# Performance work log

Hardware: AMD Instinct MI355X
Metric: run time of the kernel (lower is better)

## Reference

```python
import jax, jax.numpy as jnp
import numpy as np

B, N, D_IN, D_HID, N_ITER = 32, 512, 256, 128, 10


def setup_inputs() -> dict:
    key = jax.random.key(0)
    ks = jax.random.split(key, 8)
    s = 1.0 / np.sqrt(D_IN)  # torch Linear default init range
    return {
        "Xh": jax.random.normal(ks[0], (B, N, D_IN), jnp.float32),
        "Xm": jax.random.normal(ks[1], (B, N, D_IN), jnp.float32),
        # position 0 is the root; tokens 1..len are valid
        "lengths": jax.random.randint(ks[2], (B,), N // 2, N),
        "Wh": jax.random.uniform(ks[3], (D_HID, D_IN), jnp.float32, -s, s),
        "bh": jax.random.uniform(ks[4], (D_HID,), jnp.float32, -s, s),
        "Wm": jax.random.uniform(ks[5], (D_HID, D_IN), jnp.float32, -s, s),
        "bm": jax.random.uniform(ks[6], (D_HID,), jnp.float32, -s, s),
        "V": 0.01 * jax.random.normal(ks[7], (D_HID, D_HID), jnp.float32),
    }


def _logZ(scores, lengths):
    """Matrix-tree log-partition for single-root nonprojective trees.

    scores: [B,N,N] arc scores, scores[b,h,m] = head h -> modifier m, index 0 = root.
    lengths: [B] number of real tokens (valid modifiers at 1..len).
    """
    Bn, Nn, _ = scores.shape
    idx = jnp.arange(Nn)
    tok = (idx[None, :] >= 1) & (idx[None, :] <= lengths[:, None])   # [B,N] valid modifiers
    head = idx[None, :] <= lengths[:, None]                          # [B,N] valid heads (incl. root)
    pair = head[:, :, None] & tok[:, None, :] & (idx[:, None] != idx[None, :])
    # stability shift: every tree has exactly `len` edges, so logZ shifts by len*c
    c = jax.lax.stop_gradient(
        jnp.max(jnp.where(pair, scores, -jnp.inf), axis=(1, 2)))
    A = jnp.where(pair, jnp.exp(scores - c[:, None, None]), 0.0)     # [B,N,N]
    r = A[:, 0, 1:]                                                  # root -> token weights [B,N-1]
    At = A[:, 1:, 1:]                                                # token -> token weights
    ar = jnp.arange(Nn - 1)
    # Laplacian L = diag(colsum) - At (diag of At is zero by pair mask)
    Lap = (-At).at[:, ar, ar].set(r + At.sum(axis=1))
    # Koo et al. (2007): replace first row with root weights
    Lhat = Lap.at[:, 0, :].set(r)
    # padded positions: identity rows to keep det unchanged
    Lhat = Lhat.at[:, ar, ar].add(jnp.where(tok[:, 1:], 0.0, 1.0))
    _, logabs = jnp.linalg.slogdet(Lhat)
    return logabs + lengths.astype(scores.dtype) * c


def _marginals(scores, lengths):
    """nonprojective_marginals: (logZ, entropy, mu) via grad of logZ."""
    def f(s):
        lz = _logZ(s, lengths)
        return lz.sum(), lz
    (_, logZ), Y = jax.value_and_grad(f, has_aux=True)(scores)
    entr = logZ - jnp.sum(Y * scores, axis=(1, 2))
    return logZ, entr, Y


def reference(Xh, Xm, lengths, Wh, bh, Wm, bm, V):
    # dropout=0 -> H_mask/M_mask are ones
    H0 = Xh @ Wh.T + bh          # h_mlp(Xh), invariant across iterations
    M0 = Xm @ Wm.T + bm          # m_mlp(Xm)
    H = jax.nn.relu(H0)
    M = jax.nn.relu(M0)
    scores = jnp.einsum("bhu,uv,bmv->bhm", H, V, M)
    logZ, entr, Y = _marginals(scores, lengths)
    for _ in range(1, N_ITER):
        Hn = jax.nn.relu(H0 + Y @ M @ V.T)                       # _update_H
        Mn = jax.nn.relu(M0 + jnp.swapaxes(Y, -2, -1) @ H @ V)   # _update_M
        scores = jnp.einsum("bhu,uv,bmv->bhm", Hn, V, Mn)
        logZ, entr, Y = _marginals(scores, lengths)
        H, M = Hn, Mn
    return scores, logZ, Y, entr
```

## Files before the change

### kernel.cpp

```cpp
#include <hip/hip_runtime.h>
#include <math.h>

constexpr int BB = 32;
constexpr int NN_ = 512;
constexpr int DIN = 256;
constexpr int DH = 128;
constexpr int NITER = 10;
constexpr long HSTR = (long)NN_ * DH;
constexpr long SSTR = (long)NN_ * NN_;
constexpr long LSTR = 512L * 512L;

__device__ __forceinline__ unsigned f2mono(float f) {
    unsigned u = __float_as_uint(f);
    return (u & 0x80000000u) ? ~u : (u | 0x80000000u);
}
__device__ __forceinline__ float mono2f(unsigned u) {
    return __uint_as_float((u & 0x80000000u) ? (u & 0x7fffffffu) : ~u);
}

__device__ __forceinline__ float invert128(float r[8][8], int tid,
        float (*RowP)[8][132], float (*ColPT)[8][132], float (*Rnew)[8][132])
{
    int tx = tid & 15, ty = tid >> 4;
    int lane = tid & 63, w = tid >> 6;
    int li = lane >> 3, lj = lane & 7;
    const bool act = (tid < 256);
    float lacc = 0.f;
    __syncthreads();
    for (int s8 = 0; s8 < 16; ++s8) {
        int p = s8 & 1;
        if (act && ty == s8) {
            #pragma unroll
            for (int i = 0; i < 8; ++i)
                #pragma unroll
                for (int j = 0; j < 8; ++j)
                    RowP[p][i][tx * 8 + j] = r[i][j];
        }
        if (act && tx == s8) {
            float sub = (ty == s8) ? 1.f : 0.f;
            #pragma unroll
            for (int i = 0; i < 8; ++i)
                #pragma unroll
                for (int j = 0; j < 8; ++j)
                    ColPT[p][j][ty * 8 + i] = r[i][j] - ((i == j) ? sub : 0.f);
        }
        __syncthreads();
        float d = RowP[p][li][s8 * 8 + lj];
        float prod = 1.f;
        #pragma unroll
        for (int s = 0; s < 8; ++s) {
            float pv = __shfl(d, s * 9);
            prod *= pv;
            float pinv = 1.0f / pv;
            float rv = __shfl(d, s * 8 + lj);
            float cv = __shfl(d, li * 8 + s);
            float nd;
            if (li == s && lj == s)  nd = pinv;
            else if (li == s)        nd = rv * pinv;
            else if (lj == s)        nd = -cv * pinv;
            else                     nd = d - cv * pinv * rv;
            d = nd;
        }
        lacc += logf(fabsf(prod));
        if (act) {
            int sr = li;
            int jq = w * 32 + lj * 4;
            float dsr[8];
            #pragma unroll
            for (int t = 0; t < 8; ++t) dsr[t] = __shfl(d, (lane & 56) + t);
            float a0 = 0.f, a1 = 0.f, a2 = 0.f, a3 = 0.f;
            #pragma unroll
            for (int t = 0; t < 8; ++t) {
                float4 rp = *(const float4*)&RowP[p][t][jq];
                a0 += dsr[t] * rp.x; a1 += dsr[t] * rp.y;
                a2 += dsr[t] * rp.z; a3 += dsr[t] * rp.w;
            }
            if ((jq >> 3) == s8) {
                if ((jq & 7) == 0) {
                    a0 = dsr[0] + ((sr == 0) ? 1.f : 0.f);
                    a1 = dsr[1] + ((sr == 1) ? 1.f : 0.f);
                    a2 = dsr[2] + ((sr == 2) ? 1.f : 0.f);
                    a3 = dsr[3] + ((sr == 3) ? 1.f : 0.f);
                } else {
                    a0 = dsr[4] + ((sr == 4) ? 1.f : 0.f);
                    a1 = dsr[5] + ((sr == 5) ? 1.f : 0.f);
                    a2 = dsr[6] + ((sr == 6) ? 1.f : 0.f);
                    a3 = dsr[7] + ((sr == 7) ? 1.f : 0.f);
                }
            }
            *(float4*)&Rnew[p][sr][jq] = make_float4(a0, a1, a2, a3);
        }
        __syncthreads();
        if (act) {
            #pragma unroll
            for (int t = 0; t < 8; ++t) {
                float cp[8], rn[8];
                *(float4*)&cp[0] = *(const float4*)&ColPT[p][t][ty * 8];
                *(float4*)&cp[4] = *(const float4*)&ColPT[p][t][ty * 8 + 4];
                *(float4*)&rn[0] = *(const float4*)&Rnew[p][t][tx * 8];
                *(float4*)&rn[4] = *(const float4*)&Rnew[p][t][tx * 8 + 4];
                #pragma unroll
                for (int i = 0; i < 8; ++i)
                    #pragma unroll
                    for (int j = 0; j < 8; ++j)
                        r[i][j] -= cp[i] * rn[j];
            }
        }
    }
    return lacc;
}

template<int AMODE, int BMODE, int EPI>
__global__ __launch_bounds__(256) void gemm64(
    const float* __restrict__ A, const float* __restrict__ Bm,
    float* __restrict__ C, const float* __restrict__ Dp, float* __restrict__ C2,
    int Mdim, int Ndim, int Kdim,
    long sA, long sB, long sC, long sD)
{
    constexpr int BK = 16;
    __shared__ float As[BK][64 + 4];
    __shared__ float Bs[BK][64 + 4];
    int b = blockIdx.z;
    const float* Ab = A + (long)b * sA;
    const float* Bb = Bm + (long)b * sB;
    int m0 = blockIdx.x * 64, n0 = blockIdx.y * 64;
    int tid = threadIdx.x;
    int tx = tid & 15, ty = tid >> 4;
    float acc[4][4] = {};

    int arow, acol, brow, bcol;
    if (AMODE == 0) { arow = tid >> 2; acol = (tid & 3) * 4; }
    else            { arow = tid >> 4; acol = (tid & 15) * 4; }
    if (BMODE == 0) { brow = tid >> 4; bcol = (tid & 15) * 4; }
    else            { brow = tid >> 2; bcol = (tid & 3) * 4; }

    float4 av, bv;
    if (AMODE == 0) av = *(const float4*)(Ab + (long)(m0 + arow) * Kdim + acol);
    else            av = *(const float4*)(Ab + (long)(0 + arow) * Mdim + m0 + acol);
    if (BMODE == 0) bv = *(const float4*)(Bb + (long)(0 + brow) * Ndim + n0 + bcol);
    else            bv = *(const float4*)(Bb + (long)(n0 + brow) * Kdim + bcol);

    for (int k0 = 0; k0 < Kdim; k0 += BK) {
        __syncthreads();
        if (AMODE == 0) {
            As[acol + 0][arow] = av.x; As[acol + 1][arow] = av.y;
            As[acol + 2][arow] = av.z; As[acol + 3][arow] = av.w;
        } else {
            *(float4*)&As[arow][acol] = av;
        }
        if (BMODE == 0) {
            *(float4*)&Bs[brow][bcol] = bv;
        } else {
            Bs[bcol + 0][brow] = bv.x; Bs[bcol + 1][brow] = bv.y;
            Bs[bcol + 2][brow] = bv.z; Bs[bcol + 3][brow] = bv.w;
        }
        float4 av2, bv2;
        if (k0 + BK < Kdim) {
            int k1 = k0 + BK;
            if (AMODE == 0) av2 = *(const float4*)(Ab + (long)(m0 + arow) * Kdim + k1 + acol);
            else            av2 = *(const float4*)(Ab + (long)(k1 + arow) * Mdim + m0 + acol);
            if (BMODE == 0) bv2 = *(const float4*)(Bb + (long)(k1 + brow) * Ndim + n0 + bcol);
            else            bv2 = *(const float4*)(Bb + (long)(n0 + brow) * Kdim + k1 + bcol);
        }
        __syncthreads();
        #pragma unroll
        for (int k = 0; k < BK; ++k) {
            float4 a4 = *(const float4*)&As[k][ty * 4];
            float4 b4 = *(const float4*)&Bs[k][tx * 4];
            float avv[4] = {a4.x, a4.y, a4.z, a4.w};
            float bvv[4] = {b4.x, b4.y, b4.z, b4.w};
            #pragma unroll
            for (int i = 0; i < 4; ++i)
                #pragma unroll
                for (int j = 0; j < 4; ++j)
                    acc[i][j] += avv[i] * bvv[j];
        }
        av = av2; bv = bv2;
    }

    int r0 = m0 + ty * 4, c0 = n0 + tx * 4;
    if (EPI == 0) {
        float* Cb = C + (long)b * sC;
        #pragma unroll
        for (int i = 0; i < 4; ++i)
            *(float4*)(Cb + (long)(r0 + i) * Ndim + c0) =
                make_float4(acc[i][0], acc[i][1], acc[i][2], acc[i][3]);
    } else if (EPI == 1) {
        float4 bias = *(const float4*)(Dp + c0);
        float bb4[4] = {bias.x, bias.y, bias.z, bias.w};
        #pragma unroll
        for (int i = 0; i < 4; ++i) {
            float pre[4];
            #pragma unroll
            for (int j = 0; j < 4; ++j) pre[j] = acc[i][j] + bb4[j];
            *(float4*)(C2 + (long)(r0 + i) * Ndim + c0) =
                make_float4(pre[0], pre[1], pre[2], pre[3]);
            *(float4*)(C + (long)(r0 + i) * Ndim + c0) =
                make_float4(fmaxf(pre[0], 0.f), fmaxf(pre[1], 0.f),
                            fmaxf(pre[2], 0.f), fmaxf(pre[3], 0.f));
        }
    } else {
        const float* Db = Dp + (long)b * sD;
        float* Cb = C + (long)b * sC;
        #pragma unroll
        for (int i = 0; i < 4; ++i) {
            float4 d = *(const float4*)(Db + (long)(r0 + i) * Ndim + c0);
            float pre[4] = {acc[i][0] + d.x, acc[i][1] + d.y,
                            acc[i][2] + d.z, acc[i][3] + d.w};
            *(float4*)(Cb + (long)(r0 + i) * Ndim + c0) =
                make_float4(fmaxf(pre[0], 0.f), fmaxf(pre[1], 0.f),
                            fmaxf(pre[2], 0.f), fmaxf(pre[3], 0.f));
        }
    }
}

__global__ __launch_bounds__(256) void score_gemm(
    const float* __restrict__ A, const float* __restrict__ Bm,
    float* __restrict__ C, const int* __restrict__ len,
    unsigned* __restrict__ cu)
{
    int b = blockIdx.z;
    const float* Ab = A + (long)b * HSTR;
    const float* Bb = Bm + (long)b * HSTR;
    int m0 = blockIdx.x * 128, n0 = blockIdx.y * 128;
    int tid = threadIdx.x, tx = tid & 15, ty = tid >> 4;
    __shared__ float As[8][132];
    __shared__ float Bs[8][132];
    float acc[8][8] = {};
    int row = tid >> 1, kq = (tid & 1) << 2;
    float4 av = *(const float4*)(Ab + (long)(m0 + row) * DH + kq);
    float4 bv = *(const float4*)(Bb + (long)(n0 + row) * DH + kq);
    for (int kc = 0; kc < DH; kc += 8) {
        __syncthreads();
        As[kq + 0][row] = av.x; As[kq + 1][row] = av.y;
        As[kq + 2][row] = av.z; As[kq + 3][row] = av.w;
        Bs[kq + 0][row] = bv.x; Bs[kq + 1][row] = bv.y;
        Bs[kq + 2][row] = bv.z; Bs[kq + 3][row] = bv.w;
        float4 av2, bv2;
        if (kc + 8 < DH) {
            av2 = *(const float4*)(Ab + (long)(m0 + row) * DH + kc + 8 + kq);
            bv2 = *(const float4*)(Bb + (long)(n0 + row) * DH + kc + 8 + kq);
        }
        __syncthreads();
        #pragma unroll
        for (int k = 0; k < 8; ++k) {
            float a[8], bb[8];
            *(float4*)&a[0] = *(float4*)&As[k][ty * 8];
            *(float4*)&a[4] = *(float4*)&As[k][ty * 8 + 4];
            *(float4*)&bb[0] = *(float4*)&Bs[k][tx * 8];
            *(float4*)&bb[4] = *(float4*)&Bs[k][tx * 8 + 4];
            #pragma unroll
            for (int i = 0; i < 8; ++i)
                #pragma unroll
                for (int j = 0; j < 8; ++j) acc[i][j] += a[i] * bb[j];
        }
        av = av2; bv = bv2;
    }
    int L = len[b];
    float vmax = -3.0e38f;
    float* Cb = C + (long)b * SSTR;
    #pragma unroll
    for (int i = 0; i < 8; ++i) {
        int h = m0 + ty * 8 + i;
        bool hok = (h <= L);
        *(float4*)(Cb + (long)h * NN_ + n0 + tx * 8) =
            make_float4(acc[i][0], acc[i][1], acc[i][2], acc[i][3]);
        *(float4*)(Cb + (long)h * NN_ + n0 + tx * 8 + 4) =
            make_float4(acc[i][4], acc[i][5], acc[i][6], acc[i][7]);
        #pragma unroll
        for (int j = 0; j < 8; ++j) {
            int m = n0 + tx * 8 + j;
            if (hok && m >= 1 && m <= L && m != h) vmax = fmaxf(vmax, acc[i][j]);
        }
    }
    __syncthreads();
    float* red = &As[0][0];
    red[tid] = vmax; __syncthreads();
    for (int off = 128; off; off >>= 1) {
        if (tid < off) red[tid] = fmaxf(red[tid], red[tid + off]);
        __syncthreads();
    }
    if (tid == 0) atomicMax(&cu[b], f2mono(red[0]));
}

__global__ void zero_scal(float* scal) {
    if (threadIdx.x < 224) scal[threadIdx.x] = 0.f;
}

__global__ __launch_bounds__(256) void colsum_k(const float* __restrict__ sc,
                                                const int* __restrict__ len,
                                                const unsigned* __restrict__ cu,
                                                float* __restrict__ colsum)
{
    int b = blockIdx.x, yb = blockIdx.y;
    int tid = threadIdx.x, lane = tid & 63, w = tid >> 6;
    int L = len[b];
    float c = mono2f(cu[b]);
    int m = yb * 64 + lane;
    const float* S = sc + (long)b * SSTR;
    float s = 0.f;
    bool mv = (m >= 1 && m <= L);
    if (mv) {
        for (int h = 1 + w; h < NN_; h += 4) {
            if (h <= L && h != m) s += expf(S[(long)h * NN_ + m] - c);
        }
    }
    __shared__ float part[4][64];
    part[w][lane] = s; __syncthreads();
    if (tid < 64)
        colsum[(long)b * NN_ + yb * 64 + tid] =
            part[0][tid] + part[1][tid] + part[2][tid] + part[3][tid];
}

__global__ __launch_bounds__(256) void build_rows(const float* __restrict__ sc,
                                                  const int* __restrict__ len,
                                                  const unsigned* __restrict__ cu,
                                                  const float* __restrict__ colsum,
                                                  float* __restrict__ Lm,
                                                  float* __restrict__ Fb0,
                                                  float* __restrict__ logdet)
{
    __shared__ float sm[6][8][132];
    int b = blockIdx.x;
    int tid = threadIdx.x;
    int L = len[b];
    float c = mono2f(cu[b]);
    const float* S = sc + (long)b * SSTR;
    const float* cs = colsum + (long)b * NN_;

    if (blockIdx.y == 0) {
        int tx = tid & 15, ty = tid >> 4;
        float r[8][8];
        #pragma unroll
        for (int i = 0; i < 8; ++i) {
            int gi = ty * 8 + i;
            #pragma unroll
            for (int j = 0; j < 8; ++j) {
                int gj = tx * 8 + j;
                int tm = gj + 1;
                bool mv = (tm <= L);
                float v;
                if (gi == 0) {
                    v = mv ? expf(S[tm] - c) : 0.f;
                } else if (gi == gj) {
                    float rv = mv ? expf(S[tm] - c) : 0.f;
                    v = rv + cs[tm] + (mv ? 0.f : 1.f);
                } else {
                    int h = gi + 1;
                    v = (h <= L && mv) ? -expf(S[(long)h * NN_ + tm] - c) : 0.f;
                }
                r[i][j] = v;
            }
        }
        float lacc = invert128(r, tid,
                               (float(*)[8][132])&sm[0],
                               (float(*)[8][132])&sm[2],
                               (float(*)[8][132])&sm[4]);
        float* Ab = Lm + (long)b * LSTR;
        #pragma unroll
        for (int i = 0; i < 8; ++i) {
            *(float4*)(Ab + (long)(ty * 8 + i) * 512 + tx * 8) =
                make_float4(r[i][0], r[i][1], r[i][2], r[i][3]);
            *(float4*)(Ab + (long)(ty * 8 + i) * 512 + tx * 8 + 4) =
                make_float4(r[i][4], r[i][5], r[i][6], r[i][7]);
        }
        if (tid == 0) atomicAdd(&logdet[b], lacc);
        return;
    }

    int i0 = (blockIdx.y - 1) * 8;
    #pragma unroll
    for (int r = 0; r < 8; ++r) {
        int i = i0 + r;
        float* Lrow = Lm + (long)b * LSTR + (long)i * 512;
        float* Frow = Fb0 + (long)b * HSTR + (long)i * 128;
        #pragma unroll
        for (int q = 0; q < 2; ++q) {
            int j = tid + q * 256;
            float v;
            if (i == 511 || j == 511) {
                v = (i == j) ? 1.f : 0.f;
            } else {
                int tm = j + 1;
                bool mv = (tm <= L);
                if (i == 0) {
                    v = mv ? expf(S[tm] - c) : 0.f;
                } else if (i == j) {
                    float rv = mv ? expf(S[tm] - c) : 0.f;
                    v = rv + cs[tm] + ((tm > L) ? 1.f : 0.f);
                } else {
                    int h = i + 1;
                    v = (h <= L && mv) ? -expf(S[(long)h * NN_ + tm] - c) : 0.f;
                }
            }
            if (!(i < 128 && j < 128)) Lrow[j] = v;
            if (q == 0 && j < 128 && i >= 128) Frow[j] = v;
        }
    }
}

__global__ __launch_bounds__(256) void gj_panel(float* __restrict__ Lm,
                                                float* __restrict__ Fnext, int kb)
{
    constexpr int BK = 16;
    __shared__ float Ds[BK][132];
    __shared__ float As2[BK][36];
    int b = blockIdx.x;
    int j = blockIdx.y >> 2;
    int cq = blockIdx.y & 3;
    int jt = j + (j >= kb);
    int c0 = cq * 32;
    int tid = threadIdx.x;
    int tx = tid & 7, ty = tid >> 3;
    float* base = Lm + (long)b * LSTR;
    const float* D = base + (long)(kb * 128) * 512 + kb * 128;
    float* Aj = base + (long)(kb * 128) * 512 + jt * 128;
    int drow = tid >> 1, dk8 = (tid & 1) * 8;
    int akr = tid >> 3, acq4 = (tid & 7) * 4;
    bool aload = (akr < BK);
    float acc[4][4] = {};
    float4 dva = *(const float4*)(D + (long)drow * 512 + dk8);
    float4 dvb = *(const float4*)(D + (long)drow * 512 + dk8 + 4);
    float4 av;
    if (aload) av = *(const float4*)(Aj + (long)akr * 512 + c0 + acq4);
    for (int kc = 0; kc < 128; kc += BK) {
        __syncthreads();
        Ds[dk8 + 0][drow] = dva.x; Ds[dk8 + 1][drow] = dva.y;
        Ds[dk8 + 2][drow] = dva.z; Ds[dk8 + 3][drow] = dva.w;
        Ds[dk8 + 4][drow] = dvb.x; Ds[dk8 + 5][drow] = dvb.y;
        Ds[dk8 + 6][drow] = dvb.z; Ds[dk8 + 7][drow] = dvb.w;
        if (aload) *(float4*)&As2[akr][acq4] = av;
        float4 dva2, dvb2, av2;
        if (kc + BK < 128) {
            dva2 = *(const float4*)(D + (long)drow * 512 + kc + BK + dk8);
            dvb2 = *(const float4*)(D + (long)drow * 512 + kc + BK + dk8 + 4);
            if (aload) av2 = *(const float4*)(Aj + (long)(kc + BK + akr) * 512 + c0 + acq4);
        }
        __syncthreads();
        #pragma unroll
        for (int k = 0; k < BK; ++k) {
            float4 a4 = *(const float4*)&Ds[k][ty * 4];
            float4 b4 = *(const float4*)&As2[k][tx * 4];
            float a[4] = {a4.x, a4.y, a4.z, a4.w};
            float bb[4] = {b4.x, b4.y, b4.z, b4.w};
            #pragma unroll
            for (int i = 0; i < 4; ++i)
                #pragma unroll
                for (int jj = 0; jj < 4; ++jj)
                    acc[i][jj] += a[i] * bb[jj];
        }
        dva = dva2; dvb = dvb2; av = av2;
    }
    bool dual = (jt == kb + 1);
    float* Fn = Fnext + (long)b * HSTR + (long)(kb * 128) * 128;
    #pragma unroll
    for (int i = 0; i < 4; ++i) {
        float4 o = make_float4(acc[i][0], acc[i][1], acc[i][2], acc[i][3]);
        *(float4*)(Aj + (long)(ty * 4 + i) * 512 + c0 + tx * 4) = o;
        if (dual) *(float4*)(Fn + (long)(ty * 4 + i) * 128 + c0 + tx * 4) = o;
    }
}

__global__ __launch_bounds__(256) void gj_update64(
    float* __restrict__ Lm, const float* __restrict__ Fbuf,
    float* __restrict__ Fnext, float* __restrict__ logdet,
    unsigned* __restrict__ cnt, int kb)
{
    constexpr int BK = 16;
    __shared__ float sm[6 * 8 * 132];
    int b = blockIdx.x;
    int tid = threadIdx.x;

    if (blockIdx.z == 0) {
        if (blockIdx.y != 0 || kb >= 3) return;
        if (tid == 0) {
            while (__hip_atomic_load(&cnt[kb * 32 + b], __ATOMIC_ACQUIRE,
                                     __HIP_MEMORY_SCOPE_AGENT) < 4u) {}
        }
        __syncthreads();
        int tx = tid & 15, ty = tid >> 4;
        float* Dd = Lm + (long)b * LSTR + (long)((kb + 1) * 128) * 512 + (kb + 1) * 128;
        float r[8][8];
        #pragma unroll
        for (int i = 0; i < 8; ++i) {
            *(float4*)&r[i][0] = *(const float4*)(Dd + (long)(ty * 8 + i) * 512 + tx * 8);
            *(float4*)&r[i][4] = *(const float4*)(Dd + (long)(ty * 8 + i) * 512 + tx * 8 + 4);
        }
        float lacc = invert128(r, tid,
                               (float(*)[8][132])sm,
                               (float(*)[8][132])(sm + 2 * 8 * 132),
                               (float(*)[8][132])(sm + 4 * 8 * 132));
        #pragma unroll
        for (int i = 0; i < 8; ++i) {
            *(float4*)(Dd + (long)(ty * 8 + i) * 512 + tx * 8) =
                make_float4(r[i][0], r[i][1], r[i][2], r[i][3]);
            *(float4*)(Dd + (long)(ty * 8 + i) * 512 + tx * 8 + 4) =
                make_float4(r[i][4], r[i][5], r[i][6], r[i][7]);
        }
        if (tid == 0) atomicAdd(&logdet[b], lacc);
        return;
    }

    float (*Fs)[68] = (float (*)[68])sm;
    float (*Rs)[68] = (float (*)[68])(sm + BK * 68);
    int il = blockIdx.y;
    int it = (kb < 3) ? ((il == 0) ? kb : (il == kb ? 0 : il)) : il;
    int ib = it + (it >= kb);
    int sub = blockIdx.z - 1;
    int jl = sub >> 2;
    int jt = (kb < 3) ? ((jl == 0) ? kb + 1 : (jl == kb + 1 ? 0 : jl)) : jl;
    int quad = sub & 3;
    int r0 = (quad >> 1) * 64, c0 = (quad & 1) * 64;
    int tx = tid & 15, ty = tid >> 4;
    float* base = Lm + (long)b * LSTR;
    const float* F = Fbuf + (long)b * HSTR + (long)(ib * 128 + r0) * 128;
    const float* R = base + (long)(kb * 128) * 512 + jt * 128 + c0;
    float* Cb = base + (long)(ib * 128 + r0) * 512 + jt * 128 + c0;
    int frow = tid >> 2, fkq = (tid & 3) << 2;
    int rkr = tid >> 4, rcq = (tid & 15) << 2;
    float acc[4][4] = {};
    float4 fv = *(const float4*)(F + (long)frow * 128 + fkq);
    float4 rv = *(const float4*)(R + (long)rkr * 512 + rcq);
    for (int kc = 0; kc < 128; kc += BK) {
        __syncthreads();
        Fs[fkq + 0][frow] = fv.x; Fs[fkq + 1][frow] = fv.y;
        Fs[fkq + 2][frow] = fv.z; Fs[fkq + 3][frow] = fv.w;
        *(float4*)&Rs[rkr][rcq] = rv;
        float4 fv2, rv2;
        if (kc + BK < 128) {
            fv2 = *(const float4*)(F + (long)frow * 128 + kc + BK + fkq);
            rv2 = *(const float4*)(R + (long)(kc + BK + rkr) * 512 + rcq);
        }
        __syncthreads();
        #pragma unroll
        for (int k = 0; k < BK; ++k) {
            float4 a4 = *(const float4*)&Fs[k][ty * 4];
            float4 b4 = *(const float4*)&Rs[k][tx * 4];
            float a[4] = {a4.x, a4.y, a4.z, a4.w};
            float bb[4] = {b4.x, b4.y, b4.z, b4.w};
            #pragma unroll
            for (int i = 0; i < 4; ++i)
                #pragma unroll
                for (int j = 0; j < 4; ++j)
                    acc[i][j] += a[i] * bb[j];
        }
        fv = fv2; rv = rv2;
    }
    bool dual = (jt == kb + 1);
    float* Fn = Fnext + (long)b * HSTR + (long)(ib * 128 + r0) * 128 + c0;
    if (jt == kb) {
        #pragma unroll
        for (int i = 0; i < 4; ++i)
            *(float4*)(Cb + (long)(ty * 4 + i) * 512 + tx * 4) =
                make_float4(-acc[i][0], -acc[i][1], -acc[i][2], -acc[i][3]);
    } else {
        #pragma unroll
        for (int i = 0; i < 4; ++i) {
            float4 o = *(const float4*)(Cb + (long)(ty * 4 + i) * 512 + tx * 4);
            o = make_float4(o.x - acc[i][0], o.y - acc[i][1],
                            o.z - acc[i][2], o.w - acc[i][3]);
            *(float4*)(Cb + (long)(ty * 4 + i) * 512 + tx * 4) = o;
            if (dual) *(float4*)(Fn + (long)(ty * 4 + i) * 128 + tx * 4) = o;
        }
    }
    if (kb < 3 && ib == kb + 1 && jt == kb + 1) {
        __threadfence();
        __syncthreads();
        if (tid == 0)
            __hip_atomic_fetch_add(&cnt[kb * 32 + b], 1u, __ATOMIC_RELEASE,
                                   __HIP_MEMORY_SCOPE_AGENT);
    }
}

__global__ __launch_bounds__(256) void y_k(const float* __restrict__ sc,
                                           const float* __restrict__ Binv,
                                           const int* __restrict__ len,
                                           const unsigned* __restrict__ cu,
                                           float* __restrict__ Y,
                                           float* __restrict__ Ssum)
{
    int b = blockIdx.x;
    int ht = blockIdx.y >> 3, mt = blockIdx.y & 7;
    int h0 = ht * 64, m0 = mt * 64;
    int tid = threadIdx.x;
    int L = len[b];
    float c = mono2f(cu[b]);
    const float* S = sc + (long)b * SSTR;
    const float* Bi = Binv + (long)b * LSTR;
    float* Yb = Y + (long)b * SSTR;
    __shared__ float Bs[64][65];
    __shared__ float Ds[64], C0s[64];
    {
        int hh = tid & 63, m4 = tid >> 6;
        int col = h0 + hh - 1;
        for (int mm = m4; mm < 64; mm += 4) {
            int row = m0 + mm - 1;
            Bs[mm][hh] = (row >= 0 && col >= 0) ? Bi[(long)row * 512 + col] : 0.f;
        }
    }
    if (tid < 64) {
        int row = m0 + tid - 1;
        Ds[tid] = (row >= 0) ? Bi[(long)row * 512 + row] : 0.f;
    } else if (tid < 128) {
        int mm = tid - 64, row = m0 + mm - 1;
        C0s[mm] = (row >= 0) ? Bi[(long)row * 512] : 0.f;
    }
    __syncthreads();
    int mm = tid & 63, hq = tid >> 6;
    int m = m0 + mm;
    float lsum = 0.f;
    bool mvalid = (m >= 1 && m <= L);
    float dterm = (m >= 2) ? Ds[mm] : 0.f;
    #pragma unroll
    for (int hi = 0; hi < 16; ++hi) {
        int hh = hq * 16 + hi;
        int h = h0 + hh;
        float s = S[(long)h * NN_ + m];
        float y = 0.f;
        if (mvalid && h <= L && h != m) {
            float a = expf(s - c);
            float g;
            if (h == 0) g = C0s[mm] + dterm;
            else g = dterm - ((h >= 2) ? Bs[mm][hh] : 0.f);
            y = a * g;
        }
        Yb[(long)h * NN_ + m] = y;
        lsum += y * s;
    }
    __shared__ float red[256];
    red[tid] = lsum; __syncthreads();
    for (int off = 128; off; off >>= 1) {
        if (tid < off) red[tid] += red[tid + off];
        __syncthreads();
    }
    if (tid == 0) atomicAdd(&Ssum[b], red[0]);
}

__global__ void fin_k(const int* __restrict__ len, unsigned* __restrict__ cu,
                      float* __restrict__ logdet, float* __restrict__ Ssum,
                      unsigned* __restrict__ cnt,
                      float* __restrict__ outLogZ, float* __restrict__ outEntr)
{
    int b = threadIdx.x;
    if (b < 32) {
        float c = mono2f(cu[b]);
        float lz = logdet[b] + (float)len[b] * c;
        outLogZ[b] = lz;
        outEntr[b] = lz - Ssum[b];
        cu[b] = 0u;
        logdet[b] = 0.f;
        Ssum[b] = 0.f;
        cnt[b] = 0u;
        cnt[32 + b] = 0u;
        cnt[64 + b] = 0u;
        cnt[96 + b] = 0u;
    }
}

extern "C" void kernel_launch(void* const* d_in, const int* in_sizes, int n_in,
                              void* d_out, int out_size, void* d_ws, size_t ws_size,
                              hipStream_t stream)
{
    const float* Xh = (const float*)d_in[0];
    const float* Xm = (const float*)d_in[1];
    const int*   len = (const int*)d_in[2];
    const float* Wh = (const float*)d_in[3];
    const float* bh = (const float*)d_in[4];
    const float* Wm = (const float*)d_in[5];
    const float* bm = (const float*)d_in[6];
    const float* V  = (const float*)d_in[7];

    float* ws = (float*)d_ws;
    constexpr long U = 2097152;
    float* H0 = ws;
    float* M0 = ws + U;
    float* Ha = ws + 2 * U;
    float* Ma = ws + 3 * U;
    float* Hb = ws + 4 * U;
    float* Mb = ws + 5 * U;
    float* T1 = ws + 6 * U;
    float* Yt = ws + 7 * U;
    float* Lm = ws + 8 * U;
    float* cs = ws + 12 * U;
    float* scal = ws + 12 * U + 16384;
    unsigned* cu = (unsigned*)scal;
    float* logdet = scal + 32;
    float* Ssum = scal + 64;
    unsigned* cnt = (unsigned*)(scal + 96);

    float* Sout = (float*)d_out;
    float* outLogZ = (float*)d_out + 8388608;
    float* Yout = (float*)d_out + 8388640;
    float* outEntr = (float*)d_out + 8388640 + 8388608;

    zero_scal<<<1, 256, 0, stream>>>(scal);

    gemm64<0,1,1><<<dim3(256, 2, 1), 256, 0, stream>>>(
        Xh, Wh, Ha, bh, H0, 16384, DH, DIN, 0, 0, 0, 0);
    gemm64<0,1,1><<<dim3(256, 2, 1), 256, 0, stream>>>(
        Xm, Wm, Ma, bm, M0, 16384, DH, DIN, 0, 0, 0, 0);

    float* Hc = Ha; float* Mc = Ma; float* Hn = Hb; float* Mn = Mb;
    for (int t = 0; t < NITER; ++t) {
        if (t > 0) {
            gemm64<0,1,0><<<dim3(8,2,BB),256,0,stream>>>(
                Mc, V, Yt, nullptr, nullptr, 512, DH, DH, HSTR, 0, HSTR, 0);
            gemm64<0,0,2><<<dim3(8,2,BB),256,0,stream>>>(
                Yout, Yt, Hn, H0, nullptr, 512, DH, 512, SSTR, HSTR, HSTR, HSTR);
            gemm64<1,0,2><<<dim3(8,2,BB),256,0,stream>>>(
                Yout, T1, Mn, M0, nullptr, 512, DH, 512, SSTR, HSTR, HSTR, HSTR);
            { float* tmp = Hc; Hc = Hn; Hn = tmp; }
            { float* tmp = Mc; Mc = Mn; Mn = tmp; }
        }
        gemm64<0,0,0><<<dim3(8,2,BB),256,0,stream>>>(
            Hc, V, T1, nullptr, nullptr, 512, DH, DH, HSTR, 0, HSTR, 0);
        score_gemm<<<dim3(4,4,BB),256,0,stream>>>(T1, Mc, Sout, len, cu);

        colsum_k<<<dim3(BB,8),256,0,stream>>>(Sout, len, cu, cs);
        build_rows<<<dim3(BB,65),256,0,stream>>>(Sout, len, cu, cs, Lm, Yt, logdet);

        float* Fbufs[2] = {Yt, Hn};
        for (int kb = 0; kb < 4; ++kb) {
            float* Fcur  = Fbufs[kb & 1];
            float* Fnext = Fbufs[(kb + 1) & 1];
            gj_panel<<<dim3(BB,12),256,0,stream>>>(Lm, Fnext, kb);
            gj_update64<<<dim3(BB,3,17),256,0,stream>>>(Lm, Fcur, Fnext, logdet, cnt, kb);
        }
        y_k<<<dim3(BB,64),256,0,stream>>>(Sout, Lm, len, cu, Yout, Ssum);
        fin_k<<<1,32,0,stream>>>(len, cu, logdet, Ssum, cnt, outLogZ, outEntr);
    }
}
```

Measured before the change: 5.861 ms.

## Remove spin-wait sync in GJ update, self-compute next diag block; add 32-row update GEMM

The block-Gauss-Jordan update kernel no longer spin-waits on an atomic counter for the next diagonal tile. Instead, a dedicated block recomputes that tile itself (a 128x128x128 GEMM subtract) and then inverts it, while the other blocks skip it. The diagonal-0 build is split into its own kernel, and the H/M update GEMMs switch to a smaller 32x64 tile kernel for more blocks. This removes inter-block busy-waiting and its counters, but one block per batch now does a serial GEMM plus inversion that may sit on the critical path.

```diff
diff --git a/kernel.cpp b/kernel.cpp
--- a/kernel.cpp
+++ b/kernel.cpp
@@ -214,6 +214,86 @@
     }
 }
 
+template<int AMODE>
+__global__ __launch_bounds__(256) void gemm32(
+    const float* __restrict__ A, const float* __restrict__ Bm,
+    float* __restrict__ C, const float* __restrict__ Dp,
+    int Mdim, int Ndim, int Kdim,
+    long sA, long sB, long sC, long sD)
+{
+    constexpr int BK = 16;
+    __shared__ float As[BK][36];
+    __shared__ float Bs[BK][68];
+    int b = blockIdx.z;
+    const float* Ab = A + (long)b * sA;
+    const float* Bb = Bm + (long)b * sB;
+    int m0 = blockIdx.x * 32, n0 = blockIdx.y * 64;
+    int tid = threadIdx.x;
+    int tx = tid & 15, ty = tid >> 4;
+    float acc[2][4] = {};
+
+    int arow, acol;
+    if (AMODE == 0) { arow = tid >> 2; acol = (tid & 3) * 4; }
+    else            { arow = tid >> 3; acol = (tid & 7) * 4; }
+    bool aload = (tid < 128);
+    int brow = tid >> 4, bcol = (tid & 15) * 4;
+
+    float4 av, bv;
+    if (aload) {
+        if (AMODE == 0) av = *(const float4*)(Ab + (long)(m0 + arow) * Kdim + acol);
+        else            av = *(const float4*)(Ab + (long)arow * Mdim + m0 + acol);
+    }
+    bv = *(const float4*)(Bb + (long)brow * Ndim + n0 + bcol);
+
+    for (int k0 = 0; k0 < Kdim; k0 += BK) {
+        __syncthreads();
+        if (aload) {
+            if (AMODE == 0) {
+                As[acol + 0][arow] = av.x; As[acol + 1][arow] = av.y;
+                As[acol + 2][arow] = av.z; As[acol + 3][arow] = av.w;
+            } else {
+                *(float4*)&As[arow][acol] = av;
+            }
+        }
+        *(float4*)&Bs[brow][bcol] = bv;
+        float4 av2, bv2;
+        if (k0 + BK < Kdim) {
+            int k1 = k0 + BK;
+            if (aload) {
+                if (AMODE == 0) av2 = *(const float4*)(Ab + (long)(m0 + arow) * Kdim + k1 + acol);
+                else            av2 = *(const float4*)(Ab + (long)(k1 + arow) * Mdim + m0 + acol);
+            }
+            bv2 = *(const float4*)(Bb + (long)(k1 + brow) * Ndim + n0 + bcol);
+        }
+        __syncthreads();
+        #pragma unroll
+        for (int k = 0; k < BK; ++k) {
+            float a0 = As[k][ty * 2], a1 = As[k][ty * 2 + 1];
+            float4 b4 = *(const float4*)&Bs[k][tx * 4];
+            float bb[4] = {b4.x, b4.y, b4.z, b4.w};
+            #pragma unroll
+            for (int j = 0; j < 4; ++j) {
+                acc[0][j] += a0 * bb[j];
+                acc[1][j] += a1 * bb[j];
+            }
+        }
+        av = av2; bv = bv2;
+    }
+
+    int r0 = m0 + ty * 2, c0 = n0 + tx * 4;
+    const float* Db = Dp + (long)b * sD;
+    float* Cb = C + (long)b * sC;
+    #pragma unroll
+    for (int i = 0; i < 2; ++i) {
+        float4 d = *(const float4*)(Db + (long)(r0 + i) * Ndim + c0);
+        float pre[4] = {acc[i][0] + d.x, acc[i][1] + d.y,
+                        acc[i][2] + d.z, acc[i][3] + d.w};
+        *(float4*)(Cb + (long)(r0 + i) * Ndim + c0) =
+            make_float4(fmaxf(pre[0], 0.f), fmaxf(pre[1], 0.f),
+                        fmaxf(pre[2], 0.f), fmaxf(pre[3], 0.f));
+    }
+}
+
 __global__ __launch_bounds__(256) void score_gemm(
     const float* __restrict__ A, const float* __restrict__ Bm,
     float* __restrict__ C, const int* __restrict__ len,
@@ -284,7 +364,7 @@
 }
 
 __global__ void zero_scal(float* scal) {
-    if (threadIdx.x < 224) scal[threadIdx.x] = 0.f;
+    if (threadIdx.x < 96) scal[threadIdx.x] = 0.f;
 }
 
 __global__ __launch_bounds__(256) void colsum_k(const float* __restrict__ sc,
@@ -312,13 +392,12 @@
             part[0][tid] + part[1][tid] + part[2][tid] + part[3][tid];
 }
 
-__global__ __launch_bounds__(256) void build_rows(const float* __restrict__ sc,
-                                                  const int* __restrict__ len,
-                                                  const unsigned* __restrict__ cu,
-                                                  const float* __restrict__ colsum,
-                                                  float* __restrict__ Lm,
-                                                  float* __restrict__ Fb0,
-                                                  float* __restrict__ logdet)
+__global__ __launch_bounds__(256) void build_diag0(const float* __restrict__ sc,
+                                                   const int* __restrict__ len,
+                                                   const unsigned* __restrict__ cu,
+                                                   const float* __restrict__ colsum,
+                                                   float* __restrict__ Lm,
+                                                   float* __restrict__ logdet)
 {
     __shared__ float sm[6][8][132];
     int b = blockIdx.x;
@@ -327,48 +406,59 @@
     float c = mono2f(cu[b]);
     const float* S = sc + (long)b * SSTR;
     const float* cs = colsum + (long)b * NN_;
-
-    if (blockIdx.y == 0) {
-        int tx = tid & 15, ty = tid >> 4;
-        float r[8][8];
-        #pragma unroll
-        for (int i = 0; i < 8; ++i) {
-            int gi = ty * 8 + i;
-            #pragma unroll
-            for (int j = 0; j < 8; ++j) {
-                int gj = tx * 8 + j;
-                int tm = gj + 1;
-                bool mv = (tm <= L);
-                float v;
-                if (gi == 0) {
-                    v = mv ? expf(S[tm] - c) : 0.f;
-                } else if (gi == gj) {
-                    float rv = mv ? expf(S[tm] - c) : 0.f;
-                    v = rv + cs[tm] + (mv ? 0.f : 1.f);
-                } else {
-                    int h = gi + 1;
-                    v = (h <= L && mv) ? -expf(S[(long)h * NN_ + tm] - c) : 0.f;
-                }
-                r[i][j] = v;
-            }
-        }
-        float lacc = invert128(r, tid,
-                               (float(*)[8][132])&sm[0],
-                               (float(*)[8][132])&sm[2],
-                               (float(*)[8][132])&sm[4]);
-        float* Ab = Lm + (long)b * LSTR;
-        #pragma unroll
-        for (int i = 0; i < 8; ++i) {
-            *(float4*)(Ab + (long)(ty * 8 + i) * 512 + tx * 8) =
-                make_float4(r[i][0], r[i][1], r[i][2], r[i][3]);
-            *(float4*)(Ab + (long)(ty * 8 + i) * 512 + tx * 8 + 4) =
-                make_float4(r[i][4], r[i][5], r[i][6], r[i][7]);
-        }
-        if (tid == 0) atomicAdd(&logdet[b], lacc);
-        return;
-    }
-
-    int i0 = (blockIdx.y - 1) * 8;
+    int tx = tid & 15, ty = tid >> 4;
+    float r[8][8];
+    #pragma unroll
+    for (int i = 0; i < 8; ++i) {
+        int gi = ty * 8 + i;
+        #pragma unroll
+        for (int j = 0; j < 8; ++j) {
+            int gj = tx * 8 + j;
+            int tm = gj + 1;
+            bool mv = (tm <= L);
+            float v;
+            if (gi == 0) {
+                v = mv ? expf(S[tm] - c) : 0.f;
+            } else if (gi == gj) {
+                float rv = mv ? expf(S[tm] - c) : 0.f;
+                v = rv + cs[tm] + (mv ? 0.f : 1.f);
+            } else {
+                int h = gi + 1;
+                v = (h <= L && mv) ? -expf(S[(long)h * NN_ + tm] - c) : 0.f;
+            }
+            r[i][j] = v;
+        }
+    }
+    float lacc = invert128(r, tid,
+                           (float(*)[8][132])&sm[0],
+                           (float(*)[8][132])&sm[2],
+                           (float(*)[8][132])&sm[4]);
+    float* Ab = Lm + (long)b * LSTR;
+    #pragma unroll
+    for (int i = 0; i < 8; ++i) {
+        *(float4*)(Ab + (long)(ty * 8 + i) * 512 + tx * 8) =
+            make_float4(r[i][0], r[i][1], r[i][2], r[i][3]);
+        *(float4*)(Ab + (long)(ty * 8 + i) * 512 + tx * 8 + 4) =
+            make_float4(r[i][4], r[i][5], r[i][6], r[i][7]);
+    }
+    if (tid == 0) atomicAdd(&logdet[b], lacc);
+}
+
+__global__ __launch_bounds__(256) void build_rows(const float* __restrict__ sc,
+                                                  const int* __restrict__ len,
+                                                  const unsigned* __restrict__ cu,
+                                                  const float* __restrict__ colsum,
+                                                  float* __restrict__ Lm,
+                                                  float* __restrict__ Fb0)
+{
+    int b = blockIdx.x;
+    int tid = threadIdx.x;
+    int L = len[b];
+    float c = mono2f(cu[b]);
+    const float* S = sc + (long)b * SSTR;
+    const float* cs = colsum + (long)b * NN_;
+
+    int i0 = blockIdx.y * 8;
     #pragma unroll
     for (int r = 0; r < 8; ++r) {
         int i = i0 + r;
@@ -463,39 +553,80 @@
 
 __global__ __launch_bounds__(256) void gj_update64(
     float* __restrict__ Lm, const float* __restrict__ Fbuf,
-    float* __restrict__ Fnext, float* __restrict__ logdet,
-    unsigned* __restrict__ cnt, int kb)
+    float* __restrict__ Fnext, float* __restrict__ logdet, int kb)
 {
     constexpr int BK = 16;
     __shared__ float sm[6 * 8 * 132];
     int b = blockIdx.x;
     int tid = threadIdx.x;
+    float* base = Lm + (long)b * LSTR;
 
     if (blockIdx.z == 0) {
         if (blockIdx.y != 0 || kb >= 3) return;
-        if (tid == 0) {
-            while (__hip_atomic_load(&cnt[kb * 32 + b], __ATOMIC_ACQUIRE,
-                                     __HIP_MEMORY_SCOPE_AGENT) < 4u) {}
-        }
-        __syncthreads();
+        int dt = kb + 1;
+        const float* F = Fbuf + (long)b * HSTR + (long)(dt * 128) * 128;
+        const float* R = base + (long)(kb * 128) * 512 + dt * 128;
+        float* Cb = base + (long)(dt * 128) * 512 + dt * 128;
+        float (*Fs)[132] = (float (*)[132])sm;
+        float (*Rs)[132] = (float (*)[132])(sm + 16 * 132);
         int tx = tid & 15, ty = tid >> 4;
-        float* Dd = Lm + (long)b * LSTR + (long)((kb + 1) * 128) * 512 + (kb + 1) * 128;
-        float r[8][8];
+        int frow = tid >> 1, fkq = (tid & 1) << 3;
+        int rkr = tid >> 4, rcq = (tid & 15) << 3;
+        float acc[8][8] = {};
+        float4 fva = *(const float4*)(F + (long)frow * 128 + fkq);
+        float4 fvb = *(const float4*)(F + (long)frow * 128 + fkq + 4);
+        float4 rva = *(const float4*)(R + (long)rkr * 512 + rcq);
+        float4 rvb = *(const float4*)(R + (long)rkr * 512 + rcq + 4);
+        for (int kc = 0; kc < 128; kc += BK) {
+            __syncthreads();
+            Fs[fkq + 0][frow] = fva.x; Fs[fkq + 1][frow] = fva.y;
+            Fs[fkq + 2][frow] = fva.z; Fs[fkq + 3][frow] = fva.w;
+            Fs[fkq + 4][frow] = fvb.x; Fs[fkq + 5][frow] = fvb.y;
+            Fs[fkq + 6][frow] = fvb.z; Fs[fkq + 7][frow] = fvb.w;
+            *(float4*)&Rs[rkr][rcq] = rva;
+            *(float4*)&Rs[rkr][rcq + 4] = rvb;
+            float4 fva2, fvb2, rva2, rvb2;
+            if (kc + BK < 128) {
+                fva2 = *(const float4*)(F + (long)frow * 128 + kc + BK + fkq);
+                fvb2 = *(const float4*)(F + (long)frow * 128 + kc + BK + fkq + 4);
+                rva2 = *(const float4*)(R + (long)(kc + BK + rkr) * 512 + rcq);
+                rvb2 = *(const float4*)(R + (long)(kc + BK + rkr) * 512 + rcq + 4);
+            }
+            __syncthreads();
+            #pragma unroll
+            for (int k = 0; k < BK; ++k) {
+                float a[8], bb[8];
+                *(float4*)&a[0] = *(const float4*)&Fs[k][ty * 8];
+                *(float4*)&a[4] = *(const float4*)&Fs[k][ty * 8 + 4];
+                *(float4*)&bb[0] = *(const float4*)&Rs[k][tx * 8];
+                *(float4*)&bb[4] = *(const float4*)&Rs[k][tx * 8 + 4];
+                #pragma unroll
+                for (int i = 0; i < 8; ++i)
+                    #pragma unroll
+                    for (int j = 0; j < 8; ++j)
+                        acc[i][j] += a[i] * bb[j];
+            }
+            fva = fva2; fvb = fvb2; rva = rva2; rvb = rvb2;
+        }
         #pragma unroll
         for (int i = 0; i < 8; ++i) {
-            *(float4*)&r[i][0] = *(const float4*)(Dd + (long)(ty * 8 + i) * 512 + tx * 8);
-            *(float4*)&r[i][4] = *(const float4*)(Dd + (long)(ty * 8 + i) * 512 + tx * 8 + 4);
-        }
-        float lacc = invert128(r, tid,
-                               (float(*)[8][132])sm,
-                               (float(*)[8][132])(sm + 2 * 8 * 132),
-                               (float(*)[8][132])(sm + 4 * 8 * 132));
+            float4 o0 = *(const float4*)(Cb + (long)(ty * 8 + i) * 512 + tx * 8);
+            float4 o1 = *(const float4*)(Cb + (long)(ty * 8 + i) * 512 + tx * 8 + 4);
+            acc[i][0] = o0.x - acc[i][0]; acc[i][1] = o0.y - acc[i][1];
+            acc[i][2] = o0.z - acc[i][2]; acc[i][3] = o0.w - acc[i][3];
+            acc[i][4] = o1.x - acc[i][4]; acc[i][5] = o1.y - acc[i][5];
+            acc[i][6] = o1.z - acc[i][6]; acc[i][7] = o1.w - acc[i][7];
+        }
+        float lacc = invert128(acc, tid,
+                               (float (*)[8][132])sm,
+                               (float (*)[8][132])(sm + 2 * 8 * 132),
+                               (float (*)[8][132])(sm + 4 * 8 * 132));
         #pragma unroll
         for (int i = 0; i < 8; ++i) {
-            *(float4*)(Dd + (long)(ty * 8 + i) * 512 + tx * 8) =
-                make_float4(r[i][0], r[i][1], r[i][2], r[i][3]);
-            *(float4*)(Dd + (long)(ty * 8 + i) * 512 + tx * 8 + 4) =
-                make_float4(r[i][4], r[i][5], r[i][6], r[i][7]);
+            *(float4*)(Cb + (long)(ty * 8 + i) * 512 + tx * 8) =
+                make_float4(acc[i][0], acc[i][1], acc[i][2], acc[i][3]);
+            *(float4*)(Cb + (long)(ty * 8 + i) * 512 + tx * 8 + 4) =
+                make_float4(acc[i][4], acc[i][5], acc[i][6], acc[i][7]);
         }
         if (tid == 0) atomicAdd(&logdet[b], lacc);
         return;
@@ -503,16 +634,14 @@
 
     float (*Fs)[68] = (float (*)[68])sm;
     float (*Rs)[68] = (float (*)[68])(sm + BK * 68);
-    int il = blockIdx.y;
-    int it = (kb < 3) ? ((il == 0) ? kb : (il == kb ? 0 : il)) : il;
+    int it = blockIdx.y;
     int ib = it + (it >= kb);
     int sub = blockIdx.z - 1;
-    int jl = sub >> 2;
-    int jt = (kb < 3) ? ((jl == 0) ? kb + 1 : (jl == kb + 1 ? 0 : jl)) : jl;
+    int jt = sub >> 2;
     int quad = sub & 3;
+    if (kb < 3 && ib == kb + 1 && jt == kb + 1) return;
     int r0 = (quad >> 1) * 64, c0 = (quad & 1) * 64;
     int tx = tid & 15, ty = tid >> 4;
-    float* base = Lm + (long)b * LSTR;
     const float* F = Fbuf + (long)b * HSTR + (long)(ib * 128 + r0) * 128;
     const float* R = base + (long)(kb * 128) * 512 + jt * 128 + c0;
     float* Cb = base + (long)(ib * 128 + r0) * 512 + jt * 128 + c0;
@@ -562,13 +691,6 @@
             *(float4*)(Cb + (long)(ty * 4 + i) * 512 + tx * 4) = o;
             if (dual) *(float4*)(Fn + (long)(ty * 4 + i) * 128 + tx * 4) = o;
         }
-    }
-    if (kb < 3 && ib == kb + 1 && jt == kb + 1) {
-        __threadfence();
-        __syncthreads();
-        if (tid == 0)
-            __hip_atomic_fetch_add(&cnt[kb * 32 + b], 1u, __ATOMIC_RELEASE,
-                                   __HIP_MEMORY_SCOPE_AGENT);
     }
 }
 
@@ -638,7 +760,6 @@
 
 __global__ void fin_k(const int* __restrict__ len, unsigned* __restrict__ cu,
                       float* __restrict__ logdet, float* __restrict__ Ssum,
-                      unsigned* __restrict__ cnt,
                       float* __restrict__ outLogZ, float* __restrict__ outEntr)
 {
     int b = threadIdx.x;
@@ -650,10 +771,6 @@
         cu[b] = 0u;
         logdet[b] = 0.f;
         Ssum[b] = 0.f;
-        cnt[b] = 0u;
-        cnt[32 + b] = 0u;
-        cnt[64 + b] = 0u;
-        cnt[96 + b] = 0u;
     }
 }
 
@@ -686,14 +803,13 @@
     unsigned* cu = (unsigned*)scal;
     float* logdet = scal + 32;
     float* Ssum = scal + 64;
-    unsigned* cnt = (unsigned*)(scal + 96);
 
     float* Sout = (float*)d_out;
     float* outLogZ = (float*)d_out + 8388608;
     float* Yout = (float*)d_out + 8388640;
     float* outEntr = (float*)d_out + 8388640 + 8388608;
 
-    zero_scal<<<1, 256, 0, stream>>>(scal);
+    zero_scal<<<1, 96, 0, stream>>>(scal);
 
     gemm64<0,1,1><<<dim3(256, 2, 1), 256, 0, stream>>>(
         Xh, Wh, Ha, bh, H0, 16384, DH, DIN, 0, 0, 0, 0);
@@ -705,10 +821,10 @@
         if (t > 0) {
             gemm64<0,1,0><<<dim3(8,2,BB),256,0,stream>>>(
                 Mc, V, Yt, nullptr, nullptr, 512, DH, DH, HSTR, 0, HSTR, 0);
-            gemm64<0,0,2><<<dim3(8,2,BB),256,0,stream>>>(
-                Yout, Yt, Hn, H0, nullptr, 512, DH, 512, SSTR, HSTR, HSTR, HSTR);
-            gemm64<1,0,2><<<dim3(8,2,BB),256,0,stream>>>(
-                Yout, T1, Mn, M0, nullptr, 512, DH, 512, SSTR, HSTR, HSTR, HSTR);
+            gemm32<0><<<dim3(16,2,BB),256,0,stream>>>(
+                Yout, Yt, Hn, H0, 512, DH, 512, SSTR, HSTR, HSTR, HSTR);
+            gemm32<1><<<dim3(16,2,BB),256,0,stream>>>(
+                Yout, T1, Mn, M0, 512, DH, 512, SSTR, HSTR, HSTR, HSTR);
             { float* tmp = Hc; Hc = Hn; Hn = tmp; }
             { float* tmp = Mc; Mc = Mn; Mn = tmp; }
         }
@@ -717,16 +833,17 @@
         score_gemm<<<dim3(4,4,BB),256,0,stream>>>(T1, Mc, Sout, len, cu);
 
         colsum_k<<<dim3(BB,8),256,0,stream>>>(Sout, len, cu, cs);
-        build_rows<<<dim3(BB,65),256,0,stream>>>(Sout, len, cu, cs, Lm, Yt, logdet);
+        build_diag0<<<dim3(BB),256,0,stream>>>(Sout, len, cu, cs, Lm, logdet);
+        build_rows<<<dim3(BB,64),256,0,stream>>>(Sout, len, cu, cs, Lm, Yt);
 
         float* Fbufs[2] = {Yt, Hn};
         for (int kb = 0; kb < 4; ++kb) {
             float* Fcur  = Fbufs[kb & 1];
             float* Fnext = Fbufs[(kb + 1) & 1];
             gj_panel<<<dim3(BB,12),256,0,stream>>>(Lm, Fnext, kb);
-            gj_update64<<<dim3(BB,3,17),256,0,stream>>>(Lm, Fcur, Fnext, logdet, cnt, kb);
+            gj_update64<<<dim3(BB,3,17),256,0,stream>>>(Lm, Fcur, Fnext, logdet, kb);
         }
         y_k<<<dim3(BB,64),256,0,stream>>>(Sout, Lm, len, cu, Yout, Ssum);
-        fin_k<<<1,32,0,stream>>>(len, cu, logdet, Ssum, cnt, outLogZ, outEntr);
-    }
-}
+        fin_k<<<1,32,0,stream>>>(len, cu, logdet, Ssum, outLogZ, outEntr);
+    }
+}
```

New measurement: 5.538 ms. 5.5% less time.
